# Kernel tuning notes

Hardware: AMD Instinct MI355X
Metric: run time of the kernel (lower is better)

Reference implementation:

```python
import jax, jax.numpy as jnp
import numpy as np

EPS = 1e-12  # F.normalize default eps

def l2norm(x, axis=1):
    n = jnp.sqrt(jnp.sum(x * x, axis=axis, keepdims=True))
    return x / jnp.maximum(n, EPS)

def setup_inputs() -> dict:
    key = jax.random.key(0)
    ks = jax.random.split(key, 8)
    N, C, H, W = 32, 1024, 28, 28
    D, K, OUT = 128, 64, 1024
    return {
        "x": jax.random.normal(ks[0], (N, C, H, W), dtype=jnp.float32),
        "Wpool": jax.random.normal(ks[1], (D, C), dtype=jnp.float32) * 0.02,
        "bpool": jax.random.normal(ks[2], (D,), dtype=jnp.float32) * 0.02,
        "Wconv": jax.random.normal(ks[3], (K, D), dtype=jnp.float32) * 0.1,
        "bconv": jax.random.normal(ks[4], (K,), dtype=jnp.float32) * 0.02,
        "centroids": jax.random.uniform(ks[5], (K, D), dtype=jnp.float32),
        "Wproj": jax.random.normal(ks[6], (OUT, K * D), dtype=jnp.float32) * 0.02,
        "bproj": jax.random.normal(ks[7], (OUT,), dtype=jnp.float32) * 0.02,
    }

def reference(x, Wpool, bpool, Wconv, bconv, centroids, Wproj, bproj):
    N, C, H, W = x.shape
    K, D = centroids.shape
    S = H * W
    # 1x1 conv channel pool: (N,C,H,W) -> (N,D,H,W)
    x = jnp.einsum('nchw,dc->ndhw', x, Wpool) + bpool[None, :, None, None]
    # descriptor-wise L2 norm over channel dim
    x = l2norm(x, axis=1)
    xf = x.reshape(N, D, S)                      # (N,D,S)
    # 1x1 conv -> soft assignment logits, softmax over clusters
    sa = jnp.einsum('nds,kd->nks', xf, Wconv) + bconv[None, :, None]
    sa = jax.nn.softmax(sa, axis=1)              # (N,K,S)
    # vlad[n,k,d] = sum_s sa[n,k,s]*(xf[n,d,s] - centroids[k,d])
    #            = (sa @ xf^T) - centroids * sum_s sa   (GEMM rewrite, same math)
    vlad = jnp.einsum('nks,nds->nkd', sa, xf) - centroids[None] * jnp.sum(sa, axis=-1)[:, :, None]
    vlad = l2norm(vlad, axis=1)                  # L2Norm over dim=1 (clusters)
    vlad = vlad.reshape(N, K * D)
    vlad = vlad @ Wproj.T + bproj
    return l2norm(vlad, axis=1)
```

## Files before the change

### kernel.cpp

```cpp
#include <hip/hip_runtime.h>
#include <math.h>

#define NB 32
#define CC 1024
#define SS 784
#define SP 832
#define DD 128
#define KK 64
#define OUTD 1024
#define KD 8192
#define NSPLIT 13
#define PSPLIT 32

#define OFF_XN    0
#define OFF_SA    (OFF_XN + NB*DD*SP*2)
#define OFF_WPK   (OFF_SA + NB*KK*SP*2)
#define OFF_WCK   (OFF_WPK + 32*8*64*8*2)
#define OFF_VLADP (OFF_WCK + 16*64*8*2)
#define OFF_SASUM (OFF_VLADP + NB*NSPLIT*KD*4)
#define OFF_VLADN (OFF_SASUM + NB*NSPLIT*KK*4)
#define OFF_OUTP  (OFF_VLADN + NB*KD*4)

typedef __attribute__((ext_vector_type(8))) short bf16x8;
typedef __attribute__((ext_vector_type(4))) float f32x4;

__device__ __forceinline__ unsigned int pk_bf16(float a, float b) {
    unsigned int ua = __builtin_bit_cast(unsigned int, a);
    unsigned int ub = __builtin_bit_cast(unsigned int, b);
    ua += 0x7FFFu + ((ua >> 16) & 1u);
    ub += 0x7FFFu + ((ub >> 16) & 1u);
    return (ua >> 16) | (ub & 0xFFFF0000u);
}
__device__ __forceinline__ unsigned short f2bf(float a) {
    unsigned int ua = __builtin_bit_cast(unsigned int, a);
    ua += 0x7FFFu + ((ua >> 16) & 1u);
    return (unsigned short)(ua >> 16);
}
__device__ __forceinline__ float bf2f(unsigned short u) {
    unsigned int v = ((unsigned int)u) << 16;
    return __builtin_bit_cast(float, v);
}

__global__ __launch_bounds__(256)
void pack_weights(const float* __restrict__ Wpool, const float* __restrict__ Wconv,
                  unsigned short* __restrict__ Wpk, unsigned short* __restrict__ Wck)
{
    const int b = blockIdx.x;
    const int t = threadIdx.x;
    if (b < 8) {
#pragma unroll
        for (int i = 0; i < 8; i++) {
            const int id = t + 256 * i;
            const int ktl = id >> 9;
            const int mt  = (id >> 6) & 7;
            const int l   = id & 63;
            const int lm = l & 15, quad = l >> 4;
            const int kt = b * 4 + ktl;
            const int d = mt * 16 + lm;
            const int c = kt * 32 + quad * 8;
            const float4 v0 = *(const float4*)&Wpool[(size_t)d * CC + c];
            const float4 v1 = *(const float4*)&Wpool[(size_t)d * CC + c + 4];
            unsigned int* dst = (unsigned int*)&Wpk[(size_t)((kt * 8 + mt) * 64 + l) * 8];
            dst[0] = pk_bf16(v0.x, v0.y); dst[1] = pk_bf16(v0.z, v0.w);
            dst[2] = pk_bf16(v1.x, v1.y); dst[3] = pk_bf16(v1.z, v1.w);
        }
    } else {
#pragma unroll
        for (int i = 0; i < 4; i++) {
            const int id = t + 256 * i;
            const int tile = id >> 6;
            const int l = id & 63;
            const int lm = l & 15, quad = l >> 4;
            const int k = (tile >> 2) * 16 + lm;
            const int d = (tile & 3) * 32 + quad * 8;
            const float4 v0 = *(const float4*)&Wconv[(size_t)k * DD + d];
            const float4 v1 = *(const float4*)&Wconv[(size_t)k * DD + d + 4];
            unsigned int* dst = (unsigned int*)&Wck[(size_t)(tile * 64 + l) * 8];
            dst[0] = pk_bf16(v0.x, v0.y); dst[1] = pk_bf16(v0.z, v0.w);
            dst[2] = pk_bf16(v1.x, v1.y); dst[3] = pk_bf16(v1.z, v1.w);
        }
    }
}

__global__ __launch_bounds__(256)
void pool_norm_assign(const float* __restrict__ x, const unsigned short* __restrict__ Wpk,
                      const float* __restrict__ bpool, const unsigned short* __restrict__ Wck,
                      const float* __restrict__ bconv,
                      unsigned short* __restrict__ xn, unsigned short* __restrict__ sa)
{
    const int n  = blockIdx.y;
    const int s0 = blockIdx.x * 32;
    const int t  = threadIdx.x;
    const int l  = t & 63;
    const int w  = t >> 6;
    const int wm = w & 1;
    const int wn = w >> 1;
    const int lm = l & 15;
    const int quad = l >> 4;

    __shared__ alignas(16) unsigned short xnT[32][136];
    __shared__ float red[2][32];
    __shared__ float sums[2][2][16];

    f32x4 acc[4];
#pragma unroll
    for (int i = 0; i < 4; i++) acc[i] = (f32x4){0.f, 0.f, 0.f, 0.f};

    const float* xb = x + (size_t)n * CC * SS;
    const int s = s0 + wn * 16 + lm;
    const int s_c = (s < SS) ? s : (SS - 1);
#pragma unroll 2
    for (int kt = 0; kt < 32; kt++) {
        const float* bp = xb + (size_t)(kt * 32 + quad * 8) * SS + s_c;
        float rb[8];
#pragma unroll
        for (int j = 0; j < 8; j++) rb[j] = bp[(size_t)j * SS];
        union { unsigned int u[4]; bf16x8 v; } ub;
        ub.u[0] = pk_bf16(rb[0], rb[1]); ub.u[1] = pk_bf16(rb[2], rb[3]);
        ub.u[2] = pk_bf16(rb[4], rb[5]); ub.u[3] = pk_bf16(rb[6], rb[7]);
        const bf16x8 bfrag = ub.v;
#pragma unroll
        for (int i = 0; i < 4; i++) {
            const bf16x8 afrag = *(const bf16x8*)&Wpk[(size_t)((kt * 8 + wm * 4 + i) * 64 + l) * 8];
            acc[i] = __builtin_amdgcn_mfma_f32_16x16x32_bf16(afrag, bfrag, acc[i], 0, 0, 0);
        }
    }

    float ssq = 0.f;
#pragma unroll
    for (int i = 0; i < 4; i++) {
#pragma unroll
        for (int r = 0; r < 4; r++) {
            acc[i][r] += bpool[(wm * 4 + i) * 16 + quad * 4 + r];
            ssq += acc[i][r] * acc[i][r];
        }
    }
    ssq += __shfl_xor(ssq, 16, 64);
    ssq += __shfl_xor(ssq, 32, 64);
    if (quad == 0) red[wm][wn * 16 + lm] = ssq;
    __syncthreads();
    const int sl = wn * 16 + lm;
    const float scale = 1.f / fmaxf(sqrtf(red[0][sl] + red[1][sl]), 1e-12f);
    unsigned short* xnp = xn + (size_t)n * DD * SP;
#pragma unroll
    for (int i = 0; i < 4; i++) {
        const float v0 = acc[i][0] * scale, v1 = acc[i][1] * scale;
        const float v2 = acc[i][2] * scale, v3 = acc[i][3] * scale;
        const int dbase = (wm * 4 + i) * 16 + quad * 4;
        unsigned int* pT = (unsigned int*)&xnT[sl][dbase];
        pT[0] = pk_bf16(v0, v1);
        pT[1] = pk_bf16(v2, v3);
        xnp[(size_t)(dbase + 0) * SP + s] = f2bf(v0);
        xnp[(size_t)(dbase + 1) * SP + s] = f2bf(v1);
        xnp[(size_t)(dbase + 2) * SP + s] = f2bf(v2);
        xnp[(size_t)(dbase + 3) * SP + s] = f2bf(v3);
    }
    __syncthreads();

    const int kth = w & 1;
    const int ntA = w >> 1;
    f32x4 acc2[2];
    acc2[0] = (f32x4){0.f, 0.f, 0.f, 0.f};
    acc2[1] = (f32x4){0.f, 0.f, 0.f, 0.f};
#pragma unroll
    for (int dsv = 0; dsv < 4; dsv++) {
        const bf16x8 bfrag = *(const bf16x8*)&xnT[ntA * 16 + lm][dsv * 32 + quad * 8];
#pragma unroll
        for (int j = 0; j < 2; j++) {
            const int tile = ((kth * 2 + j) * 4 + dsv);
            const bf16x8 afrag = *(const bf16x8*)&Wck[(size_t)(tile * 64 + l) * 8];
            acc2[j] = __builtin_amdgcn_mfma_f32_16x16x32_bf16(afrag, bfrag, acc2[j], 0, 0, 0);
        }
    }
    float ex[2][4]; float psum = 0.f;
#pragma unroll
    for (int j = 0; j < 2; j++)
#pragma unroll
        for (int r = 0; r < 4; r++) {
            const int k = (kth * 2 + j) * 16 + quad * 4 + r;
            const float e = expf(acc2[j][r] + bconv[k]);
            ex[j][r] = e; psum += e;
        }
    psum += __shfl_xor(psum, 16, 64);
    psum += __shfl_xor(psum, 32, 64);
    if (quad == 0) sums[kth][ntA][lm] = psum;
    __syncthreads();
    const float inv = 1.f / (sums[0][ntA][lm] + sums[1][ntA][lm]);
    const int s2 = s0 + ntA * 16 + lm;
    const bool val2 = s2 < SS;
    unsigned short* sap = sa + (size_t)n * KK * SP;
#pragma unroll
    for (int j = 0; j < 2; j++)
#pragma unroll
        for (int r = 0; r < 4; r++) {
            const int k = (kth * 2 + j) * 16 + quad * 4 + r;
            sap[(size_t)k * SP + s2] = val2 ? f2bf(ex[j][r] * inv) : (unsigned short)0;
        }
}

__global__ __launch_bounds__(256)
void vlad_mfma(const unsigned short* __restrict__ xn, const unsigned short* __restrict__ sa,
               float* __restrict__ vladp, float* __restrict__ sasump)
{
    const int p = blockIdx.x;
    const int n = blockIdx.y;
    const int t = threadIdx.x;
    const int l = t & 63;
    const int w = t >> 6;
    const int kth = w & 1, nh = w >> 1;
    const int lm = l & 15, quad = l >> 4;

    const unsigned short* sap = sa + (size_t)n * KK * SP;
    const unsigned short* xnp = xn + (size_t)n * DD * SP;

    f32x4 acc[2][4];
#pragma unroll
    for (int j = 0; j < 2; j++)
#pragma unroll
        for (int i = 0; i < 4; i++) acc[j][i] = (f32x4){0.f, 0.f, 0.f, 0.f};

#pragma unroll
    for (int st = 0; st < 2; st++) {
        const int sb = p * 64 + st * 32 + quad * 8;
        bf16x8 af[2], bfv[4];
#pragma unroll
        for (int j = 0; j < 2; j++)
            af[j] = *(const bf16x8*)&sap[(size_t)((kth * 2 + j) * 16 + lm) * SP + sb];
#pragma unroll
        for (int i = 0; i < 4; i++)
            bfv[i] = *(const bf16x8*)&xnp[(size_t)((nh * 4 + i) * 16 + lm) * SP + sb];
#pragma unroll
        for (int j = 0; j < 2; j++)
#pragma unroll
            for (int i = 0; i < 4; i++)
                acc[j][i] = __builtin_amdgcn_mfma_f32_16x16x32_bf16(af[j], bfv[i], acc[j][i], 0, 0, 0);
    }

    float* vp = vladp + ((size_t)n * NSPLIT + p) * KD;
#pragma unroll
    for (int j = 0; j < 2; j++)
#pragma unroll
        for (int i = 0; i < 4; i++) {
            const int kq = (kth * 2 + j) * 4 + quad;
            const int d  = (nh * 4 + i) * 16 + lm;
            *(f32x4*)&vp[(size_t)(kq * DD + d) * 4] = acc[j][i];
        }

    if (t < KK) {
        float sm = 0.f;
        const unsigned short* rp = &sap[(size_t)t * SP + p * 64];
#pragma unroll
        for (int c = 0; c < 64; c++) sm += bf2f(rp[c]);
        sasump[((size_t)n * NSPLIT + p) * KK + t] = sm;
    }
}

__global__ __launch_bounds__(256)
void vlad_finish(const float* __restrict__ vladp, const float* __restrict__ sasump,
                 const float* __restrict__ centroids, float* __restrict__ vladn)
{
    const int dg = blockIdx.x;
    const int n  = blockIdx.y;
    const int t  = threadIdx.x;
    const int d  = dg * 8 + (t >> 5);
    const int k0 = (t & 31) * 2;

    __shared__ float sas[KK];
    if (t < KK) {
        float sm = 0.f;
#pragma unroll
        for (int p = 0; p < NSPLIT; p++) sm += sasump[((size_t)n * NSPLIT + p) * KK + t];
        sas[t] = sm;
    }
    __syncthreads();

    const int kq = k0 >> 2, r0 = k0 & 3;
    float v0 = 0.f, v1 = 0.f;
#pragma unroll
    for (int p = 0; p < NSPLIT; p++) {
        const float2 pr = *(const float2*)&vladp[((size_t)n * NSPLIT + p) * KD + (size_t)(kq * DD + d) * 4 + r0];
        v0 += pr.x; v1 += pr.y;
    }
    v0 -= centroids[(size_t)k0 * DD + d] * sas[k0];
    v1 -= centroids[(size_t)(k0 + 1) * DD + d] * sas[k0 + 1];

    float ssq = v0 * v0 + v1 * v1;
    ssq += __shfl_xor(ssq, 1, 64);
    ssq += __shfl_xor(ssq, 2, 64);
    ssq += __shfl_xor(ssq, 4, 64);
    ssq += __shfl_xor(ssq, 8, 64);
    ssq += __shfl_xor(ssq, 16, 64);
    const float scale = 1.f / fmaxf(sqrtf(ssq), 1e-12f);

    float* vo = vladn + (size_t)n * KD;
    vo[(size_t)k0 * DD + d]       = v0 * scale;
    vo[(size_t)(k0 + 1) * DD + d] = v1 * scale;
}

__global__ __launch_bounds__(256)
void proj_partial_kernel(const float* __restrict__ vladn, const float* __restrict__ Wproj,
                         float* __restrict__ outp)
{
    const int o0 = blockIdx.x * 64;
    const int c0 = blockIdx.y * (KD / PSPLIT);
    const int t  = threadIdx.x;
    const int ow = t & 31, nw = t >> 5;
    const int wr = t & 63, wq = t >> 6;
    const int vr = t & 31, vq = t >> 5;

    __shared__ float Ws[64][33];
    __shared__ float Vs[32][33];

    float acc[2][4];
#pragma unroll
    for (int i = 0; i < 2; i++)
#pragma unroll
        for (int j = 0; j < 4; j++) acc[i][j] = 0.f;

    float4 w0 = *(const float4*)&Wproj[(size_t)(o0 + wr) * KD + c0 + wq * 8];
    float4 w1 = *(const float4*)&Wproj[(size_t)(o0 + wr) * KD + c0 + wq * 8 + 4];
    float4 v4 = *(const float4*)&vladn[(size_t)vr * KD + c0 + vq * 4];

    for (int cc0 = c0; cc0 < c0 + KD / PSPLIT; cc0 += 32) {
        Ws[wr][wq * 8 + 0] = w0.x; Ws[wr][wq * 8 + 1] = w0.y;
        Ws[wr][wq * 8 + 2] = w0.z; Ws[wr][wq * 8 + 3] = w0.w;
        Ws[wr][wq * 8 + 4] = w1.x; Ws[wr][wq * 8 + 5] = w1.y;
        Ws[wr][wq * 8 + 6] = w1.z; Ws[wr][wq * 8 + 7] = w1.w;
        Vs[vr][vq * 4 + 0] = v4.x; Vs[vr][vq * 4 + 1] = v4.y;
        Vs[vr][vq * 4 + 2] = v4.z; Vs[vr][vq * 4 + 3] = v4.w;
        __syncthreads();
        if (cc0 + 32 < c0 + KD / PSPLIT) {
            w0 = *(const float4*)&Wproj[(size_t)(o0 + wr) * KD + cc0 + 32 + wq * 8];
            w1 = *(const float4*)&Wproj[(size_t)(o0 + wr) * KD + cc0 + 32 + wq * 8 + 4];
            v4 = *(const float4*)&vladn[(size_t)vr * KD + cc0 + 32 + vq * 4];
        }
#pragma unroll
        for (int cc = 0; cc < 32; cc++) {
            float wv[2], vv[4];
            wv[0] = Ws[ow][cc]; wv[1] = Ws[ow + 32][cc];
#pragma unroll
            for (int j = 0; j < 4; j++) vv[j] = Vs[nw + 8 * j][cc];
#pragma unroll
            for (int i = 0; i < 2; i++)
#pragma unroll
                for (int j = 0; j < 4; j++) acc[i][j] += wv[i] * vv[j];
        }
        __syncthreads();
    }

#pragma unroll
    for (int i = 0; i < 2; i++)
#pragma unroll
        for (int j = 0; j < 4; j++) {
            const int o = o0 + ow + 32 * i;
            const int nn = nw + 8 * j;
            outp[((size_t)blockIdx.y * NB + nn) * OUTD + o] = acc[i][j];
        }
}

__global__ __launch_bounds__(256)
void final_norm_kernel(const float* __restrict__ outp, const float* __restrict__ bproj,
                       float* __restrict__ out)
{
    const int n = blockIdx.x;
    const int t = threadIdx.x;
    const int o4 = t * 4;

    float4 a = *(const float4*)&bproj[o4];
#pragma unroll
    for (int p = 0; p < PSPLIT; p++) {
        const float4 pr = *(const float4*)&outp[((size_t)p * NB + n) * OUTD + o4];
        a.x += pr.x; a.y += pr.y; a.z += pr.z; a.w += pr.w;
    }
    float ssp = a.x * a.x + a.y * a.y + a.z * a.z + a.w * a.w;
#pragma unroll
    for (int off = 32; off > 0; off >>= 1) ssp += __shfl_down(ssp, off, 64);
    __shared__ float rs[4];
    if ((t & 63) == 0) rs[t >> 6] = ssp;
    __syncthreads();
    const float total = rs[0] + rs[1] + rs[2] + rs[3];
    const float scale = 1.f / fmaxf(sqrtf(total), 1e-12f);
    float4 o;
    o.x = a.x * scale; o.y = a.y * scale; o.z = a.z * scale; o.w = a.w * scale;
    *(float4*)&out[(size_t)n * OUTD + o4] = o;
}

extern "C" void kernel_launch(void* const* d_in, const int* in_sizes, int n_in,
                              void* d_out, int out_size, void* d_ws, size_t ws_size,
                              hipStream_t stream)
{
    const float* x         = (const float*)d_in[0];
    const float* Wpool     = (const float*)d_in[1];
    const float* bpool     = (const float*)d_in[2];
    const float* Wconv     = (const float*)d_in[3];
    const float* bconv     = (const float*)d_in[4];
    const float* centroids = (const float*)d_in[5];
    const float* Wproj     = (const float*)d_in[6];
    const float* bproj     = (const float*)d_in[7];
    float* out = (float*)d_out;
    char*  wsb = (char*)d_ws;

    unsigned short* xn     = (unsigned short*)(wsb + OFF_XN);
    unsigned short* sa     = (unsigned short*)(wsb + OFF_SA);
    unsigned short* Wpk    = (unsigned short*)(wsb + OFF_WPK);
    unsigned short* Wck    = (unsigned short*)(wsb + OFF_WCK);
    float*          vladp  = (float*)(wsb + OFF_VLADP);
    float*          sasump = (float*)(wsb + OFF_SASUM);
    float*          vladn  = (float*)(wsb + OFF_VLADN);
    float*          outp   = (float*)(wsb + OFF_OUTP);

    pack_weights<<<dim3(9), 256, 0, stream>>>(Wpool, Wconv, Wpk, Wck);
    pool_norm_assign<<<dim3(SP / 32, NB), 256, 0, stream>>>(x, Wpk, bpool, Wck, bconv, xn, sa);
    vlad_mfma<<<dim3(NSPLIT, NB), 256, 0, stream>>>(xn, sa, vladp, sasump);
    vlad_finish<<<dim3(16, NB), 256, 0, stream>>>(vladp, sasump, centroids, vladn);
    proj_partial_kernel<<<dim3(OUTD / 64, PSPLIT), 256, 0, stream>>>(vladn, Wproj, outp);
    final_norm_kernel<<<dim3(NB), 256, 0, stream>>>(outp, bproj, out);
}
```

Measured before the change: 253.0 us.

## Stage x tile in LDS, vectorize vlad_finish, move projection GEMM to bf16 MFMA

The pooling kernel now uses 16-column tiles. It stages the whole bf16-converted x slab into shared memory once, so each x element is read by one thread instead of by both M-waves, and it prefetches the Wpool fragments. vlad_finish handles four clusters per thread with vector loads. The FP32 LDS-tiled projection is replaced by a bf16 MFMA kernel that reads Wproj and vladn directly. This trades some projection precision and doubles the pooling grid.

```diff
diff --git a/kernel.cpp b/kernel.cpp
--- a/kernel.cpp
+++ b/kernel.cpp
@@ -89,113 +89,113 @@
                       unsigned short* __restrict__ xn, unsigned short* __restrict__ sa)
 {
     const int n  = blockIdx.y;
-    const int s0 = blockIdx.x * 32;
+    const int s0 = blockIdx.x * 16;
     const int t  = threadIdx.x;
     const int l  = t & 63;
     const int w  = t >> 6;
-    const int wm = w & 1;
-    const int wn = w >> 1;
     const int lm = l & 15;
     const int quad = l >> 4;
 
-    __shared__ alignas(16) unsigned short xnT[32][136];
-    __shared__ float red[2][32];
-    __shared__ float sums[2][2][16];
-
-    f32x4 acc[4];
-#pragma unroll
-    for (int i = 0; i < 4; i++) acc[i] = (f32x4){0.f, 0.f, 0.f, 0.f};
-
-    const float* xb = x + (size_t)n * CC * SS;
-    const int s = s0 + wn * 16 + lm;
-    const int s_c = (s < SS) ? s : (SS - 1);
-#pragma unroll 2
+    __shared__ alignas(16) unsigned short Bst[128 * 16 * 8];
+    __shared__ alignas(16) unsigned short xnT[16 * 16 * 8];
+    __shared__ float red[4][16];
+    __shared__ float sums[4][16];
+
+    {
+        const int s_l = t & 15;
+        const int cb0 = t >> 4;
+        const int sg  = s0 + s_l;
+        const int s_c = (sg < SS) ? sg : (SS - 1);
+        const float* xb = x + (size_t)n * CC * SS + s_c;
+#pragma unroll
+        for (int it = 0; it < 8; it++) {
+            const int cblk = cb0 + 16 * it;
+            const float* xp = xb + (size_t)(cblk * 8) * SS;
+            float v[8];
+#pragma unroll
+            for (int j = 0; j < 8; j++) v[j] = xp[(size_t)j * SS];
+            unsigned int* dst = (unsigned int*)&Bst[(size_t)(cblk * 16 + s_l) * 8];
+            dst[0] = pk_bf16(v[0], v[1]); dst[1] = pk_bf16(v[2], v[3]);
+            dst[2] = pk_bf16(v[4], v[5]); dst[3] = pk_bf16(v[6], v[7]);
+        }
+    }
+    __syncthreads();
+
+    f32x4 acc[2];
+    acc[0] = (f32x4){0.f, 0.f, 0.f, 0.f};
+    acc[1] = (f32x4){0.f, 0.f, 0.f, 0.f};
+
+    bf16x8 a_nxt[2];
+#pragma unroll
+    for (int i = 0; i < 2; i++)
+        a_nxt[i] = *(const bf16x8*)&Wpk[(size_t)((0 * 8 + w * 2 + i) * 64 + l) * 8];
+
     for (int kt = 0; kt < 32; kt++) {
-        const float* bp = xb + (size_t)(kt * 32 + quad * 8) * SS + s_c;
-        float rb[8];
-#pragma unroll
-        for (int j = 0; j < 8; j++) rb[j] = bp[(size_t)j * SS];
-        union { unsigned int u[4]; bf16x8 v; } ub;
-        ub.u[0] = pk_bf16(rb[0], rb[1]); ub.u[1] = pk_bf16(rb[2], rb[3]);
-        ub.u[2] = pk_bf16(rb[4], rb[5]); ub.u[3] = pk_bf16(rb[6], rb[7]);
-        const bf16x8 bfrag = ub.v;
-#pragma unroll
-        for (int i = 0; i < 4; i++) {
-            const bf16x8 afrag = *(const bf16x8*)&Wpk[(size_t)((kt * 8 + wm * 4 + i) * 64 + l) * 8];
-            acc[i] = __builtin_amdgcn_mfma_f32_16x16x32_bf16(afrag, bfrag, acc[i], 0, 0, 0);
-        }
-    }
-
+        const bf16x8 a0 = a_nxt[0], a1 = a_nxt[1];
+        if (kt < 31) {
+#pragma unroll
+            for (int i = 0; i < 2; i++)
+                a_nxt[i] = *(const bf16x8*)&Wpk[(size_t)(((kt + 1) * 8 + w * 2 + i) * 64 + l) * 8];
+        }
+        const bf16x8 bfrag = *(const bf16x8*)&Bst[(size_t)((kt * 4 + quad) * 16 + lm) * 8];
+        acc[0] = __builtin_amdgcn_mfma_f32_16x16x32_bf16(a0, bfrag, acc[0], 0, 0, 0);
+        acc[1] = __builtin_amdgcn_mfma_f32_16x16x32_bf16(a1, bfrag, acc[1], 0, 0, 0);
+    }
+
+    float vals[2][4];
     float ssq = 0.f;
 #pragma unroll
-    for (int i = 0; i < 4; i++) {
+    for (int i = 0; i < 2; i++)
 #pragma unroll
         for (int r = 0; r < 4; r++) {
-            acc[i][r] += bpool[(wm * 4 + i) * 16 + quad * 4 + r];
-            ssq += acc[i][r] * acc[i][r];
-        }
-    }
+            const int d = (w * 2 + i) * 16 + quad * 4 + r;
+            const float v = acc[i][r] + bpool[d];
+            vals[i][r] = v; ssq += v * v;
+        }
     ssq += __shfl_xor(ssq, 16, 64);
     ssq += __shfl_xor(ssq, 32, 64);
-    if (quad == 0) red[wm][wn * 16 + lm] = ssq;
-    __syncthreads();
-    const int sl = wn * 16 + lm;
-    const float scale = 1.f / fmaxf(sqrtf(red[0][sl] + red[1][sl]), 1e-12f);
+    if (quad == 0) red[w][lm] = ssq;
+    __syncthreads();
+    const float scale = 1.f / fmaxf(sqrtf(red[0][lm] + red[1][lm] + red[2][lm] + red[3][lm]), 1e-12f);
+    const int sg = s0 + lm;
     unsigned short* xnp = xn + (size_t)n * DD * SP;
 #pragma unroll
-    for (int i = 0; i < 4; i++) {
-        const float v0 = acc[i][0] * scale, v1 = acc[i][1] * scale;
-        const float v2 = acc[i][2] * scale, v3 = acc[i][3] * scale;
-        const int dbase = (wm * 4 + i) * 16 + quad * 4;
-        unsigned int* pT = (unsigned int*)&xnT[sl][dbase];
-        pT[0] = pk_bf16(v0, v1);
-        pT[1] = pk_bf16(v2, v3);
-        xnp[(size_t)(dbase + 0) * SP + s] = f2bf(v0);
-        xnp[(size_t)(dbase + 1) * SP + s] = f2bf(v1);
-        xnp[(size_t)(dbase + 2) * SP + s] = f2bf(v2);
-        xnp[(size_t)(dbase + 3) * SP + s] = f2bf(v3);
-    }
-    __syncthreads();
-
-    const int kth = w & 1;
-    const int ntA = w >> 1;
-    f32x4 acc2[2];
-    acc2[0] = (f32x4){0.f, 0.f, 0.f, 0.f};
-    acc2[1] = (f32x4){0.f, 0.f, 0.f, 0.f};
+    for (int i = 0; i < 2; i++)
+#pragma unroll
+        for (int r = 0; r < 4; r++) {
+            const int d = (w * 2 + i) * 16 + quad * 4 + r;
+            const float v = vals[i][r] * scale;
+            xnp[(size_t)d * SP + sg] = f2bf(v);
+            xnT[(size_t)(((d >> 3) * 16) + lm) * 8 + (d & 7)] = f2bf(v);
+        }
+    __syncthreads();
+
+    f32x4 acc2 = (f32x4){0.f, 0.f, 0.f, 0.f};
 #pragma unroll
     for (int dsv = 0; dsv < 4; dsv++) {
-        const bf16x8 bfrag = *(const bf16x8*)&xnT[ntA * 16 + lm][dsv * 32 + quad * 8];
-#pragma unroll
-        for (int j = 0; j < 2; j++) {
-            const int tile = ((kth * 2 + j) * 4 + dsv);
-            const bf16x8 afrag = *(const bf16x8*)&Wck[(size_t)(tile * 64 + l) * 8];
-            acc2[j] = __builtin_amdgcn_mfma_f32_16x16x32_bf16(afrag, bfrag, acc2[j], 0, 0, 0);
-        }
-    }
-    float ex[2][4]; float psum = 0.f;
-#pragma unroll
-    for (int j = 0; j < 2; j++)
-#pragma unroll
-        for (int r = 0; r < 4; r++) {
-            const int k = (kth * 2 + j) * 16 + quad * 4 + r;
-            const float e = expf(acc2[j][r] + bconv[k]);
-            ex[j][r] = e; psum += e;
-        }
-    psum += __shfl_xor(psum, 16, 64);
-    psum += __shfl_xor(psum, 32, 64);
-    if (quad == 0) sums[kth][ntA][lm] = psum;
-    __syncthreads();
-    const float inv = 1.f / (sums[0][ntA][lm] + sums[1][ntA][lm]);
-    const int s2 = s0 + ntA * 16 + lm;
-    const bool val2 = s2 < SS;
+        const bf16x8 bfrag = *(const bf16x8*)&xnT[(size_t)((dsv * 4 + quad) * 16 + lm) * 8];
+        const bf16x8 afrag = *(const bf16x8*)&Wck[(size_t)((w * 4 + dsv) * 64 + l) * 8];
+        acc2 = __builtin_amdgcn_mfma_f32_16x16x32_bf16(afrag, bfrag, acc2, 0, 0, 0);
+    }
+    float e[4]; float ps = 0.f;
+#pragma unroll
+    for (int r = 0; r < 4; r++) {
+        const int k = w * 16 + quad * 4 + r;
+        e[r] = expf(acc2[r] + bconv[k]);
+        ps += e[r];
+    }
+    ps += __shfl_xor(ps, 16, 64);
+    ps += __shfl_xor(ps, 32, 64);
+    if (quad == 0) sums[w][lm] = ps;
+    __syncthreads();
+    const float inv = 1.f / (sums[0][lm] + sums[1][lm] + sums[2][lm] + sums[3][lm]);
+    const bool val2 = sg < SS;
     unsigned short* sap = sa + (size_t)n * KK * SP;
 #pragma unroll
-    for (int j = 0; j < 2; j++)
-#pragma unroll
-        for (int r = 0; r < 4; r++) {
-            const int k = (kth * 2 + j) * 16 + quad * 4 + r;
-            sap[(size_t)k * SP + s2] = val2 ? f2bf(ex[j][r] * inv) : (unsigned short)0;
-        }
+    for (int r = 0; r < 4; r++) {
+        const int k = w * 16 + quad * 4 + r;
+        sap[(size_t)k * SP + sg] = val2 ? f2bf(e[r] * inv) : (unsigned short)0;
+    }
 }
 
 __global__ __launch_bounds__(256)
@@ -262,8 +262,8 @@
     const int dg = blockIdx.x;
     const int n  = blockIdx.y;
     const int t  = threadIdx.x;
-    const int d  = dg * 8 + (t >> 5);
-    const int k0 = (t & 31) * 2;
+    const int kq = t & 15;
+    const int d  = dg * 16 + (t >> 4);
 
     __shared__ float sas[KK];
     if (t < KK) {
@@ -274,87 +274,71 @@
     }
     __syncthreads();
 
-    const int kq = k0 >> 2, r0 = k0 & 3;
-    float v0 = 0.f, v1 = 0.f;
+    f32x4 v = (f32x4){0.f, 0.f, 0.f, 0.f};
 #pragma unroll
     for (int p = 0; p < NSPLIT; p++) {
-        const float2 pr = *(const float2*)&vladp[((size_t)n * NSPLIT + p) * KD + (size_t)(kq * DD + d) * 4 + r0];
-        v0 += pr.x; v1 += pr.y;
-    }
-    v0 -= centroids[(size_t)k0 * DD + d] * sas[k0];
-    v1 -= centroids[(size_t)(k0 + 1) * DD + d] * sas[k0 + 1];
-
-    float ssq = v0 * v0 + v1 * v1;
+        const f32x4 pr = *(const f32x4*)&vladp[((size_t)n * NSPLIT + p) * KD + (size_t)(kq * DD + d) * 4];
+        v += pr;
+    }
+#pragma unroll
+    for (int r = 0; r < 4; r++)
+        v[r] -= centroids[(size_t)(kq * 4 + r) * DD + d] * sas[kq * 4 + r];
+
+    float ssq = v[0] * v[0] + v[1] * v[1] + v[2] * v[2] + v[3] * v[3];
     ssq += __shfl_xor(ssq, 1, 64);
     ssq += __shfl_xor(ssq, 2, 64);
     ssq += __shfl_xor(ssq, 4, 64);
     ssq += __shfl_xor(ssq, 8, 64);
-    ssq += __shfl_xor(ssq, 16, 64);
     const float scale = 1.f / fmaxf(sqrtf(ssq), 1e-12f);
 
     float* vo = vladn + (size_t)n * KD;
-    vo[(size_t)k0 * DD + d]       = v0 * scale;
-    vo[(size_t)(k0 + 1) * DD + d] = v1 * scale;
-}
-
-__global__ __launch_bounds__(256)
-void proj_partial_kernel(const float* __restrict__ vladn, const float* __restrict__ Wproj,
-                         float* __restrict__ outp)
+#pragma unroll
+    for (int r = 0; r < 4; r++)
+        vo[(size_t)(kq * 4 + r) * DD + d] = v[r] * scale;
+}
+
+__global__ __launch_bounds__(256)
+void proj_mfma(const float* __restrict__ vladn, const float* __restrict__ Wproj,
+               float* __restrict__ outp)
 {
     const int o0 = blockIdx.x * 64;
     const int c0 = blockIdx.y * (KD / PSPLIT);
     const int t  = threadIdx.x;
-    const int ow = t & 31, nw = t >> 5;
-    const int wr = t & 63, wq = t >> 6;
-    const int vr = t & 31, vq = t >> 5;
-
-    __shared__ float Ws[64][33];
-    __shared__ float Vs[32][33];
-
-    float acc[2][4];
-#pragma unroll
-    for (int i = 0; i < 2; i++)
-#pragma unroll
-        for (int j = 0; j < 4; j++) acc[i][j] = 0.f;
-
-    float4 w0 = *(const float4*)&Wproj[(size_t)(o0 + wr) * KD + c0 + wq * 8];
-    float4 w1 = *(const float4*)&Wproj[(size_t)(o0 + wr) * KD + c0 + wq * 8 + 4];
-    float4 v4 = *(const float4*)&vladn[(size_t)vr * KD + c0 + vq * 4];
-
-    for (int cc0 = c0; cc0 < c0 + KD / PSPLIT; cc0 += 32) {
-        Ws[wr][wq * 8 + 0] = w0.x; Ws[wr][wq * 8 + 1] = w0.y;
-        Ws[wr][wq * 8 + 2] = w0.z; Ws[wr][wq * 8 + 3] = w0.w;
-        Ws[wr][wq * 8 + 4] = w1.x; Ws[wr][wq * 8 + 5] = w1.y;
-        Ws[wr][wq * 8 + 6] = w1.z; Ws[wr][wq * 8 + 7] = w1.w;
-        Vs[vr][vq * 4 + 0] = v4.x; Vs[vr][vq * 4 + 1] = v4.y;
-        Vs[vr][vq * 4 + 2] = v4.z; Vs[vr][vq * 4 + 3] = v4.w;
-        __syncthreads();
-        if (cc0 + 32 < c0 + KD / PSPLIT) {
-            w0 = *(const float4*)&Wproj[(size_t)(o0 + wr) * KD + cc0 + 32 + wq * 8];
-            w1 = *(const float4*)&Wproj[(size_t)(o0 + wr) * KD + cc0 + 32 + wq * 8 + 4];
-            v4 = *(const float4*)&vladn[(size_t)vr * KD + cc0 + 32 + vq * 4];
-        }
-#pragma unroll
-        for (int cc = 0; cc < 32; cc++) {
-            float wv[2], vv[4];
-            wv[0] = Ws[ow][cc]; wv[1] = Ws[ow + 32][cc];
-#pragma unroll
-            for (int j = 0; j < 4; j++) vv[j] = Vs[nw + 8 * j][cc];
-#pragma unroll
-            for (int i = 0; i < 2; i++)
-#pragma unroll
-                for (int j = 0; j < 4; j++) acc[i][j] += wv[i] * vv[j];
-        }
-        __syncthreads();
-    }
-
-#pragma unroll
-    for (int i = 0; i < 2; i++)
-#pragma unroll
-        for (int j = 0; j < 4; j++) {
-            const int o = o0 + ow + 32 * i;
-            const int nn = nw + 8 * j;
-            outp[((size_t)blockIdx.y * NB + nn) * OUTD + o] = acc[i][j];
+    const int l  = t & 63;
+    const int w  = t >> 6;
+    const int lm = l & 15, quad = l >> 4;
+    const int o  = o0 + w * 16 + lm;
+
+    f32x4 acc[2];
+    acc[0] = (f32x4){0.f, 0.f, 0.f, 0.f};
+    acc[1] = (f32x4){0.f, 0.f, 0.f, 0.f};
+
+#pragma unroll 2
+    for (int kt = 0; kt < 8; kt++) {
+        const int c = c0 + kt * 32 + quad * 8;
+        const float4 b0 = *(const float4*)&Wproj[(size_t)o * KD + c];
+        const float4 b1 = *(const float4*)&Wproj[(size_t)o * KD + c + 4];
+        float4 a00 = *(const float4*)&vladn[(size_t)(0 * 16 + lm) * KD + c];
+        float4 a01 = *(const float4*)&vladn[(size_t)(0 * 16 + lm) * KD + c + 4];
+        float4 a10 = *(const float4*)&vladn[(size_t)(16 + lm) * KD + c];
+        float4 a11 = *(const float4*)&vladn[(size_t)(16 + lm) * KD + c + 4];
+        union { unsigned int u[4]; bf16x8 v; } ub, ua0, ua1;
+        ub.u[0] = pk_bf16(b0.x, b0.y); ub.u[1] = pk_bf16(b0.z, b0.w);
+        ub.u[2] = pk_bf16(b1.x, b1.y); ub.u[3] = pk_bf16(b1.z, b1.w);
+        ua0.u[0] = pk_bf16(a00.x, a00.y); ua0.u[1] = pk_bf16(a00.z, a00.w);
+        ua0.u[2] = pk_bf16(a01.x, a01.y); ua0.u[3] = pk_bf16(a01.z, a01.w);
+        ua1.u[0] = pk_bf16(a10.x, a10.y); ua1.u[1] = pk_bf16(a10.z, a10.w);
+        ua1.u[2] = pk_bf16(a11.x, a11.y); ua1.u[3] = pk_bf16(a11.z, a11.w);
+        acc[0] = __builtin_amdgcn_mfma_f32_16x16x32_bf16(ua0.v, ub.v, acc[0], 0, 0, 0);
+        acc[1] = __builtin_amdgcn_mfma_f32_16x16x32_bf16(ua1.v, ub.v, acc[1], 0, 0, 0);
+    }
+
+#pragma unroll
+    for (int a = 0; a < 2; a++)
+#pragma unroll
+        for (int r = 0; r < 4; r++) {
+            const int nn = a * 16 + quad * 4 + r;
+            outp[((size_t)blockIdx.y * NB + nn) * OUTD + o] = acc[a][r];
         }
 }
 
@@ -410,9 +394,9 @@
     float*          outp   = (float*)(wsb + OFF_OUTP);
 
     pack_weights<<<dim3(9), 256, 0, stream>>>(Wpool, Wconv, Wpk, Wck);
-    pool_norm_assign<<<dim3(SP / 32, NB), 256, 0, stream>>>(x, Wpk, bpool, Wck, bconv, xn, sa);
+    pool_norm_assign<<<dim3(SP / 16, NB), 256, 0, stream>>>(x, Wpk, bpool, Wck, bconv, xn, sa);
     vlad_mfma<<<dim3(NSPLIT, NB), 256, 0, stream>>>(xn, sa, vladp, sasump);
-    vlad_finish<<<dim3(16, NB), 256, 0, stream>>>(vladp, sasump, centroids, vladn);
-    proj_partial_kernel<<<dim3(OUTD / 64, PSPLIT), 256, 0, stream>>>(vladn, Wproj, outp);
+    vlad_finish<<<dim3(DD / 16, NB), 256, 0, stream>>>(vladp, sasump, centroids, vladn);
+    proj_mfma<<<dim3(OUTD / 64, PSPLIT), 256, 0, stream>>>(vladn, Wproj, outp);
     final_norm_kernel<<<dim3(NB), 256, 0, stream>>>(outp, bproj, out);
 }
```

Result: faster. 234.3 us (-7.4%).
